# Kernel tuning notes

Hardware: AMD Instinct MI355X
Metric: run time of the kernel (lower is better)

## Reference

```python
import jax, jax.numpy as jnp
import numpy as np

B, C_IN, C_OUT, HID, HW = 128, 1024, 1024, 256, 32

def setup_inputs() -> dict:
    key = jax.random.key(0)
    ks = jax.random.split(key, 5)
    inp = {
        "input": jax.random.normal(ks[0], (B, C_IN, HW, HW), dtype=jnp.float32),
        "fc1_w": jax.random.normal(ks[1], (HID, C_IN), dtype=jnp.float32) * 0.02,
        "fc1_b": jnp.ones((HID,), dtype=jnp.float32),
        "fc2_w": jax.random.normal(ks[2], (C_OUT, HID), dtype=jnp.float32) * (np.sqrt(2.0 / HID)),
        "fc2_b": jnp.ones((C_OUT,), dtype=jnp.float32),
        "noise": jax.random.normal(ks[3], (B, C_OUT), dtype=jnp.float32),
        "swap_idx": jax.random.randint(ks[4], (C_OUT // 2,), 0, B, dtype=jnp.int64 if jax.config.read('jax_enable_x64') else jnp.int32),
    }
    return inp

def reference(input, fc1_w, fc1_b, fc2_w, fc2_b, noise, swap_idx):
    # global average pool over H, W -> [B, C_in]
    x = jnp.mean(input, axis=(2, 3))
    y = jax.nn.relu(x @ fc1_w.T + fc1_b)          # [B, HID]
    y2 = y @ fc2_w.T + fc2_b                      # [B, C_out]
    g = noise + y2
    v1 = jnp.clip(1.2 * jax.nn.sigmoid(g) - 0.1, 0.0, 1.0)
    v2 = (g > 0).astype(v1.dtype)
    # semhash: overwrite random batch rows of v1 with hard-binarized v2
    swapped = v1.at[swap_idx].set(v2[swap_idx])
    # straight-through: forward uses swapped values, backward is identity w.r.t. v1
    out = v1 + jax.lax.stop_gradient(swapped - v1)
    return out[:, :, None, None]                  # [B, C_out, 1, 1]
```

## Files before the change

### kernel.cpp

```cpp
#include <hip/hip_runtime.h>
#include <cstdint>

#define NB    128
#define NCIN  1024
#define NCOUT 1024
#define NHID  256
#define NHW   1024

typedef float f32x4 __attribute__((ext_vector_type(4)));

__global__ __launch_bounds__(256) void gap_kernel(const float* __restrict__ in,
                                                  float* __restrict__ x) {
    __shared__ float part[16][65];
    const int w    = threadIdx.x >> 6;
    const int lane = threadIdx.x & 63;
    const int rowBase = blockIdx.x * 16;
    const f32x4* base = reinterpret_cast<const f32x4*>(in);

    f32x4 v[4][4];
#pragma unroll
    for (int r = 0; r < 4; ++r) {
        const f32x4* p = base + (size_t)(rowBase + w * 4 + r) * (NHW / 4);
#pragma unroll
        for (int k = 0; k < 4; ++k)
            v[r][k] = __builtin_nontemporal_load(p + lane + 64 * k);
    }
#pragma unroll
    for (int r = 0; r < 4; ++r) {
        float t0 = (v[r][0].x + v[r][0].y) + (v[r][0].z + v[r][0].w);
        float t1 = (v[r][1].x + v[r][1].y) + (v[r][1].z + v[r][1].w);
        float t2 = (v[r][2].x + v[r][2].y) + (v[r][2].z + v[r][2].w);
        float t3 = (v[r][3].x + v[r][3].y) + (v[r][3].z + v[r][3].w);
        part[w * 4 + r][lane] = (t0 + t1) + (t2 + t3);
    }
    __syncthreads();

    const int row = threadIdx.x >> 4;
    const int seg = threadIdx.x & 15;
    double s = ((double)part[row][seg * 4 + 0] + (double)part[row][seg * 4 + 1])
             + ((double)part[row][seg * 4 + 2] + (double)part[row][seg * 4 + 3]);
    s += __shfl_xor(s, 1, 64);
    s += __shfl_xor(s, 2, 64);
    s += __shfl_xor(s, 4, 64);
    s += __shfl_xor(s, 8, 64);
    if (seg == 0) x[rowBase + row] = (float)(s * (1.0 / 1024.0));
}

__global__ __launch_bounds__(256) void fc1_kernel(const float* __restrict__ x,
                                                  const float* __restrict__ w1,
                                                  const float* __restrict__ b1,
                                                  float* __restrict__ y) {
    __shared__ float4 xs4[8][33];
    const int b  = blockIdx.x >> 3;
    const int ho = blockIdx.x & 7;
    const int t  = threadIdx.x;

    {
        float4 v = reinterpret_cast<const float4*>(x + (size_t)b * NCIN)[t];
        xs4[t >> 5][t & 31] = v;
    }
    __syncthreads();

    const int hl = t >> 3;
    const int cs = t & 7;
    const int h  = ho * 32 + hl;
    const float4* w = reinterpret_cast<const float4*>(w1 + (size_t)h * NCIN + cs * 128);
    double a0 = 0.0, a1 = 0.0, a2 = 0.0, a3 = 0.0;
#pragma unroll
    for (int i = 0; i < 32; ++i) {
        float4 wv = w[i];
        float4 xv = xs4[cs][i];
        a0 += (double)wv.x * (double)xv.x;
        a1 += (double)wv.y * (double)xv.y;
        a2 += (double)wv.z * (double)xv.z;
        a3 += (double)wv.w * (double)xv.w;
    }
    double s = (a0 + a1) + (a2 + a3);
    s += __shfl_xor(s, 1, 64);
    s += __shfl_xor(s, 2, 64);
    s += __shfl_xor(s, 4, 64);
    if (cs == 0) {
        double v = s + (double)b1[h];
        y[(size_t)b * NHID + h] = (float)(v > 0.0 ? v : 0.0);
    }
}

__global__ __launch_bounds__(256) void fc2_kernel(const float* __restrict__ y,
                                                  const float* __restrict__ w2,
                                                  const float* __restrict__ b2,
                                                  const float* __restrict__ noise,
                                                  const int* __restrict__ swap_idx,
                                                  int n_swap,
                                                  float* __restrict__ out) {
    __shared__ float ys[NHID];
    __shared__ int flag;
    const int b  = blockIdx.x >> 3;
    const int jo = blockIdx.x & 7;
    const int t  = threadIdx.x;

    if (t == 0) flag = 0;
    ys[t] = y[(size_t)b * NHID + t];
    __syncthreads();
    for (int i = t; i < n_swap; i += 256)
        if (swap_idx[i] == b) flag = 1;
    __syncthreads();
    const bool sw = (flag != 0);

    const int jl = t >> 1;
    const int ch = t & 1;
    const int j  = jo * 128 + jl;
    const float4* w  = reinterpret_cast<const float4*>(w2 + (size_t)j * NHID + ch * 128);
    const float*  yp = ys + ch * 128;
    double a0 = 0.0, a1 = 0.0, a2 = 0.0, a3 = 0.0;
#pragma unroll
    for (int i = 0; i < 32; ++i) {
        float4 wv = w[i];
        a0 += (double)wv.x * (double)yp[4 * i + 0];
        a1 += (double)wv.y * (double)yp[4 * i + 1];
        a2 += (double)wv.z * (double)yp[4 * i + 2];
        a3 += (double)wv.w * (double)yp[4 * i + 3];
    }
    double s = (a0 + a1) + (a2 + a3);
    s += __shfl_xor(s, 1, 64);
    if (ch == 0) {
        double g = s + (double)b2[j] + (double)noise[(size_t)b * NCOUT + j];
        float gf  = (float)g;
        float sig = 1.0f / (1.0f + __expf(-gf));
        float v1  = fminf(fmaxf(1.2f * sig - 0.1f, 0.0f), 1.0f);
        float v2  = (g > 0.0) ? 1.0f : 0.0f;
        out[(size_t)b * NCOUT + j] = sw ? v2 : v1;
    }
}

extern "C" void kernel_launch(void* const* d_in, const int* in_sizes, int n_in,
                              void* d_out, int out_size, void* d_ws, size_t ws_size,
                              hipStream_t stream) {
    const float* input = (const float*)d_in[0];
    const float* fc1_w = (const float*)d_in[1];
    const float* fc1_b = (const float*)d_in[2];
    const float* fc2_w = (const float*)d_in[3];
    const float* fc2_b = (const float*)d_in[4];
    const float* noise = (const float*)d_in[5];
    const int*   swap  = (const int*)d_in[6];
    const int n_swap = in_sizes[6];

    float* x = (float*)d_ws;
    float* y = x + NB * NCIN;

    gap_kernel<<<(NB * NCIN) / 16, 256, 0, stream>>>(input, x);
    fc1_kernel<<<NB * 8, 256, 0, stream>>>(x, fc1_w, fc1_b, y);
    fc2_kernel<<<NB * 8, 256, 0, stream>>>(y, fc2_w, fc2_b, noise, swap, n_swap,
                                           (float*)d_out);
}
```

Baseline: 120.5 us.

## Rewrite global-average-pool as grid-stride persistent waves with shuffle-only reduction

The pooling kernel now launches a fixed grid of 2048 blocks. Each wave loops over pairs of rows, reduces them in registers with a float wave-shuffle tree and writes both results with one float2 store. This removes the shared-memory staging, the __syncthreads and the double-precision final reduction, and cuts the launch from 8192 blocks to 2048. The risks are fewer bytes in flight per wave per iteration and slightly different float rounding from dropping the double accumulation.

New measurement: 118.0 us. 1.02x faster.

```diff
diff --git a/kernel.cpp b/kernel.cpp
--- a/kernel.cpp
+++ b/kernel.cpp
@@ -7,43 +7,46 @@
 #define NHID  256
 #define NHW   1024
 
+#define GAP_BLOCKS 2048
+#define GAP_WAVES  (GAP_BLOCKS * 4)
+#define GAP_ITERS  (NB * NCIN / (GAP_WAVES * 2))
+
 typedef float f32x4 __attribute__((ext_vector_type(4)));
 
 __global__ __launch_bounds__(256) void gap_kernel(const float* __restrict__ in,
                                                   float* __restrict__ x) {
-    __shared__ float part[16][65];
-    const int w    = threadIdx.x >> 6;
+    const int gw   = (blockIdx.x * 256 + threadIdx.x) >> 6;
     const int lane = threadIdx.x & 63;
-    const int rowBase = blockIdx.x * 16;
     const f32x4* base = reinterpret_cast<const f32x4*>(in);
 
-    f32x4 v[4][4];
 #pragma unroll
-    for (int r = 0; r < 4; ++r) {
-        const f32x4* p = base + (size_t)(rowBase + w * 4 + r) * (NHW / 4);
+    for (int i = 0; i < GAP_ITERS; ++i) {
+        const int row = (i * GAP_WAVES + gw) * 2;
+        const f32x4* p = base + (size_t)row * (NHW / 4);
+        f32x4 a0 = __builtin_nontemporal_load(p + lane);
+        f32x4 a1 = __builtin_nontemporal_load(p + lane + 64);
+        f32x4 a2 = __builtin_nontemporal_load(p + lane + 128);
+        f32x4 a3 = __builtin_nontemporal_load(p + lane + 192);
+        f32x4 b0 = __builtin_nontemporal_load(p + lane + 256);
+        f32x4 b1 = __builtin_nontemporal_load(p + lane + 320);
+        f32x4 b2 = __builtin_nontemporal_load(p + lane + 384);
+        f32x4 b3 = __builtin_nontemporal_load(p + lane + 448);
+
+        float s0 = (((a0.x + a0.y) + (a0.z + a0.w)) + ((a1.x + a1.y) + (a1.z + a1.w)))
+                 + (((a2.x + a2.y) + (a2.z + a2.w)) + ((a3.x + a3.y) + (a3.z + a3.w)));
+        float s1 = (((b0.x + b0.y) + (b0.z + b0.w)) + ((b1.x + b1.y) + (b1.z + b1.w)))
+                 + (((b2.x + b2.y) + (b2.z + b2.w)) + ((b3.x + b3.y) + (b3.z + b3.w)));
+
 #pragma unroll
-        for (int k = 0; k < 4; ++k)
-            v[r][k] = __builtin_nontemporal_load(p + lane + 64 * k);
+        for (int off = 1; off <= 32; off <<= 1) {
+            s0 += __shfl_xor(s0, off, 64);
+            s1 += __shfl_xor(s1, off, 64);
+        }
+        if (lane == 0) {
+            float2 r = { s0 * (1.0f / 1024.0f), s1 * (1.0f / 1024.0f) };
+            *reinterpret_cast<float2*>(x + row) = r;
+        }
     }
-#pragma unroll
-    for (int r = 0; r < 4; ++r) {
-        float t0 = (v[r][0].x + v[r][0].y) + (v[r][0].z + v[r][0].w);
-        float t1 = (v[r][1].x + v[r][1].y) + (v[r][1].z + v[r][1].w);
-        float t2 = (v[r][2].x + v[r][2].y) + (v[r][2].z + v[r][2].w);
-        float t3 = (v[r][3].x + v[r][3].y) + (v[r][3].z + v[r][3].w);
-        part[w * 4 + r][lane] = (t0 + t1) + (t2 + t3);
-    }
-    __syncthreads();
-
-    const int row = threadIdx.x >> 4;
-    const int seg = threadIdx.x & 15;
-    double s = ((double)part[row][seg * 4 + 0] + (double)part[row][seg * 4 + 1])
-             + ((double)part[row][seg * 4 + 2] + (double)part[row][seg * 4 + 3]);
-    s += __shfl_xor(s, 1, 64);
-    s += __shfl_xor(s, 2, 64);
-    s += __shfl_xor(s, 4, 64);
-    s += __shfl_xor(s, 8, 64);
-    if (seg == 0) x[rowBase + row] = (float)(s * (1.0 / 1024.0));
 }
 
 __global__ __launch_bounds__(256) void fc1_kernel(const float* __restrict__ x,
@@ -147,7 +150,7 @@
     float* x = (float*)d_ws;
     float* y = x + NB * NCIN;
 
-    gap_kernel<<<(NB * NCIN) / 16, 256, 0, stream>>>(input, x);
+    gap_kernel<<<GAP_BLOCKS, 256, 0, stream>>>(input, x);
     fc1_kernel<<<NB * 8, 256, 0, stream>>>(x, fc1_w, fc1_b, y);
     fc2_kernel<<<NB * 8, 256, 0, stream>>>(y, fc2_w, fc2_b, noise, swap, n_swap,
                                            (float*)d_out);
```
